# Performance work log

Measured on AMD Instinct MI355X. Metric: run time of the kernel, lower is better.

The kernel has to match this reference:

```python
import jax, jax.numpy as jnp
import numpy as np

N_NODES = 131072
N_EDGES = 2097152
B = 256
NODES_PER_GRAPH = 512  # uniform graphs -> to_dense_batch == reshape
F_IN = 74
D = 128
L = 3
EPS = 1e-5


def setup_inputs() -> dict:
    key = jax.random.key(0)
    ks = jax.random.split(key, 12)
    x = jax.random.normal(ks[0], (N_NODES, F_IN), dtype=jnp.float32)
    edge_index = jax.random.randint(ks[1], (2, N_EDGES), 0, N_NODES, dtype=jnp.int32)
    batch = (jnp.arange(N_NODES, dtype=jnp.int32) // NODES_PER_GRAPH)
    s = 1.0 / np.sqrt(D)
    W_init = jax.random.uniform(ks[2], (F_IN, D), jnp.float32, -s, s)
    W_gcn = jax.random.uniform(ks[3], (L, D, D), jnp.float32, -s, s)
    b_gcn = jnp.zeros((L, D), jnp.float32)
    gamma = jnp.ones((L, D), jnp.float32)
    beta = jnp.zeros((L, D), jnp.float32)
    W_res = jax.random.uniform(ks[4], (L, D, D), jnp.float32, -s, s)
    b_res = jax.random.uniform(ks[5], (L, D), jnp.float32, -s, s)
    return {"x": x, "edge_index": edge_index, "batch": batch, "W_init": W_init,
            "W_gcn": W_gcn, "b_gcn": b_gcn, "gamma": gamma, "beta": beta,
            "W_res": W_res, "b_res": b_res}


def _gcn_conv(x, src, tgt, norm, W, b):
    # PyG GCNConv: h = x @ W ; out[tgt] += norm * h[src] ; + bias
    h = x @ W                                    # [N, D]
    msg = h[src] * norm[:, None]                 # [E+N, D] gather (memory-bound)
    out = jax.ops.segment_sum(msg, tgt, num_segments=N_NODES)
    return out + b


def _batchnorm(x, g, bta):
    mean = jnp.mean(x, axis=0)
    var = jnp.var(x, axis=0)  # biased, matches torch BN training forward
    return (x - mean) * jax.lax.rsqrt(var + EPS) * g + bta


def reference(x, edge_index, batch, W_init, W_gcn, b_gcn, gamma, beta, W_res, b_res):
    # add self loops once; symmetric deg^{-1/2} normalization (PyG default)
    loops = jnp.arange(N_NODES, dtype=edge_index.dtype)
    src = jnp.concatenate([edge_index[0], loops])
    tgt = jnp.concatenate([edge_index[1], loops])
    deg = jax.ops.segment_sum(jnp.ones_like(src, dtype=jnp.float32), tgt,
                              num_segments=N_NODES)
    dinv = jnp.where(deg > 0, jax.lax.rsqrt(jnp.maximum(deg, 1.0)), 0.0)
    norm = dinv[src] * dinv[tgt]

    h = x @ W_init                               # init_transform (no bias)
    for i in range(L):
        conv = _gcn_conv(h, src, tgt, norm, W_gcn[i], b_gcn[i])
        h_new = jax.nn.relu(_batchnorm(conv, gamma[i], beta[i]))
        h = h_new + (h @ W_res[i] + b_res[i])
    # to_dense_batch with uniform NODES_PER_GRAPH -> reshape, all mask=True
    return h.reshape(B, NODES_PER_GRAPH, D)
```

## Files before the change

### kernel.cpp

```cpp
#include <hip/hip_runtime.h>

#define NN 131072
#define NE 2097152
#define DD 128
#define LL 3

#define NB 256
#define BSH 9
#define TILE (NE / NB)

typedef __attribute__((ext_vector_type(8))) short short8;
typedef __attribute__((ext_vector_type(4))) float f32x4;

__device__ __forceinline__ ushort f2bf(float f) {
    uint u = __float_as_uint(f);
    return (ushort)((u + 0x7fffu + ((u >> 16) & 1u)) >> 16);
}
__device__ __forceinline__ float bflo(uint u) { return __uint_as_float(u << 16); }
__device__ __forceinline__ float bfhi(uint u) { return __uint_as_float(u & 0xffff0000u); }

__global__ __launch_bounds__(256) void k_zero(float* __restrict__ bns) {
    int i = blockIdx.x * 256 + threadIdx.x;
    if (i < 768) bns[i] = 0.0f;
}

__global__ __launch_bounds__(256) void kA_count(const int* __restrict__ tgt,
                                                int* __restrict__ blockHist) {
    __shared__ int hist[NB];
    const int t = threadIdx.x, blk = blockIdx.x;
    hist[t] = 0;
    __syncthreads();
    const int base = blk * TILE;
#pragma unroll 8
    for (int j = 0; j < TILE / 256; ++j)
        atomicAdd(&hist[tgt[base + j * 256 + t] >> BSH], 1);
    __syncthreads();
    blockHist[t * NB + blk] = hist[t];
}

__global__ __launch_bounds__(256) void kA_scan(int* __restrict__ blockHist,
                                               int* __restrict__ bstart) {
    __shared__ int part[NB];
    const int t = threadIdx.x;
    int4* bh = (int4*)(blockHist + t * NB);
    int run = 0;
    int4 tmp[NB / 4];
#pragma unroll 8
    for (int j = 0; j < NB / 4; ++j) tmp[j] = bh[j];
#pragma unroll 8
    for (int j = 0; j < NB / 4; ++j) {
        int4 v = tmp[j];
        int a = run; run += v.x;
        int b = run; run += v.y;
        int c = run; run += v.z;
        int d = run; run += v.w;
        tmp[j] = make_int4(a, b, c, d);
    }
    part[t] = run;
    __syncthreads();
    for (int off = 1; off < NB; off <<= 1) {
        int v = part[t];
        int u = (t >= off) ? part[t - off] : 0;
        __syncthreads();
        part[t] = v + u;
        __syncthreads();
    }
    const int excl = part[t] - run;
    bstart[t] = excl;
    if (t == NB - 1) bstart[NB] = part[t];
#pragma unroll 8
    for (int j = 0; j < NB / 4; ++j) {
        int4 v = tmp[j];
        bh[j] = make_int4(v.x + excl, v.y + excl, v.z + excl, v.w + excl);
    }
}

__global__ __launch_bounds__(256) void kA_scatter(const int* __restrict__ src,
                                                  const int* __restrict__ tgt,
                                                  const int* __restrict__ chunkBase,
                                                  uint* __restrict__ packed) {
    __shared__ int cur[NB];
    const int t = threadIdx.x, blk = blockIdx.x;
    cur[t] = chunkBase[t * NB + blk];
    __syncthreads();
    const int base = blk * TILE;
#pragma unroll 4
    for (int j = 0; j < TILE / 256; ++j) {
        const int e = base + j * 256 + t;
        const int tg = tgt[e], s = src[e];
        const int b = tg >> BSH;
        const int pos = atomicAdd(&cur[b], 1);
        packed[pos] = (uint)s | ((uint)(tg & ((1 << BSH) - 1)) << 17);
    }
}

__global__ __launch_bounds__(256) void kB_sort(const uint* __restrict__ packed,
                                               const int* __restrict__ bstart,
                                               int* __restrict__ rowp,
                                               float* __restrict__ dinv,
                                               int* __restrict__ ssrc) {
    __shared__ int cnt[1 << BSH];
    __shared__ int pscan[256];
    const int t = threadIdx.x, b = blockIdx.x;
    const int e0 = bstart[b], e1 = bstart[b + 1];
    cnt[t] = 0; cnt[t + 256] = 0;
    __syncthreads();
    for (int e = e0 + t; e < e1; e += 256)
        atomicAdd(&cnt[packed[e] >> 17], 1);
    __syncthreads();
    const int c0 = cnt[2 * t], c1 = cnt[2 * t + 1];
    pscan[t] = c0 + c1;
    __syncthreads();
    for (int off = 1; off < 256; off <<= 1) {
        int v = pscan[t];
        int u = (t >= off) ? pscan[t - off] : 0;
        __syncthreads();
        pscan[t] = v + u;
        __syncthreads();
    }
    const int ex0 = pscan[t] - c0 - c1;
    const int ex1 = ex0 + c0;
    const int n0 = (b << BSH) + 2 * t;
    rowp[n0] = e0 + ex0;
    rowp[n0 + 1] = e0 + ex1;
    dinv[n0] = rsqrtf((float)(c0 + 1));
    dinv[n0 + 1] = rsqrtf((float)(c1 + 1));
    if (b == NB - 1 && t == 255) rowp[NN] = e1;
    __syncthreads();
    cnt[2 * t] = ex0;
    cnt[2 * t + 1] = ex1;
    __syncthreads();
    for (int e = e0 + t; e < e1; e += 256) {
        const uint p = packed[e];
        const int pos = atomicAdd(&cnt[p >> 17], 1);
        ssrc[e0 + pos] = (int)(p & 0x1FFFFu);
    }
}

__global__ __launch_bounds__(256) void k_prepw(const float* __restrict__ Wi,
                                               const float* __restrict__ Wg,
                                               const float* __restrict__ Wr,
                                               ushort* __restrict__ wt) {
    const int id = blockIdx.x * 256 + threadIdx.x;
    const int m = id >> 14;
    const int c = (id >> 7) & 127;
    const int k = id & 127;
    float v;
    if (m == 0)      v = (k < 74) ? Wi[k * DD + c] : 0.0f;
    else if (m <= 3) v = Wg[(size_t)(m - 1) * DD * DD + k * DD + c];
    else             v = Wr[(size_t)(m - 4) * DD * DD + k * DD + c];
    wt[id] = f2bf(v);
}

__global__ __launch_bounds__(256) void k_convx(const float* __restrict__ x,
                                               uint* __restrict__ xb) {
    const size_t id = (size_t)blockIdx.x * 256 + threadIdx.x;
    const int n = (int)(id >> 6);
    const int k0 = (int)(id & 63) * 2;
    float v0 = (k0 < 74) ? x[(size_t)n * 74 + k0] : 0.0f;
    float v1 = (k0 + 1 < 74) ? x[(size_t)n * 74 + k0 + 1] : 0.0f;
    xb[id] = (uint)f2bf(v0) | ((uint)f2bf(v1) << 16);
}

template <int MODE>
__global__ __launch_bounds__(256) void k_mgemm(const ushort* A,
                                               const ushort* __restrict__ Bt,
                                               ushort* outb,
                                               float* __restrict__ outf,
                                               const float* __restrict__ conv,
                                               const float* __restrict__ ss,
                                               const float* __restrict__ bres,
                                               float* __restrict__ bnsums) {
    __shared__ ushort As[16384];
    __shared__ ushort Bs[16384];
    __shared__ float sred[256];
    const int t = threadIdx.x;
    const int w = t >> 6, l = t & 63;
    const int lc = l & 15, lr = l >> 4;
    const size_t row0 = (size_t)blockIdx.x * 128;

    for (int ch = w * 8; ch < w * 8 + 8; ++ch) {
        const int row = ch * 4 + lr;
        const int kb = (lc * 16) ^ ((row & 7) << 4);
        const ushort* srcA = A + (row0 + row) * DD + (kb >> 1);
        const ushort* srcB = Bt + (size_t)row * DD + (kb >> 1);
        __builtin_amdgcn_global_load_lds(
            (const __attribute__((address_space(1))) void*)srcA,
            (__attribute__((address_space(3))) void*)(As + ch * 512), 16, 0, 0);
        __builtin_amdgcn_global_load_lds(
            (const __attribute__((address_space(1))) void*)srcB,
            (__attribute__((address_space(3))) void*)(Bs + ch * 512), 16, 0, 0);
    }
    if (MODE == 1) sred[t] = 0.0f;
    __syncthreads();

    f32x4 acc[2][8] = {};
    const char* Ab = (const char*)As;
    const char* Bb = (const char*)Bs;
#pragma unroll
    for (int kk = 0; kk < 4; ++kk) {
        const int kb = kk * 64 + lr * 16;
        short8 a[2];
#pragma unroll
        for (int m = 0; m < 2; ++m) {
            const int r = w * 32 + m * 16 + lc;
            a[m] = *(const short8*)(Ab + r * 256 + (kb ^ ((r & 7) << 4)));
        }
#pragma unroll
        for (int n = 0; n < 8; ++n) {
            const int c = n * 16 + lc;
            short8 b = *(const short8*)(Bb + c * 256 + (kb ^ ((c & 7) << 4)));
            acc[0][n] = __builtin_amdgcn_mfma_f32_16x16x32_bf16(a[0], b, acc[0][n], 0, 0, 0);
            acc[1][n] = __builtin_amdgcn_mfma_f32_16x16x32_bf16(a[1], b, acc[1][n], 0, 0, 0);
        }
    }

    if (MODE == 0) {
#pragma unroll
        for (int m = 0; m < 2; ++m)
#pragma unroll
            for (int n = 0; n < 8; ++n) {
                const int c = n * 16 + lc;
#pragma unroll
                for (int j = 0; j < 4; ++j) {
                    const size_t r = row0 + w * 32 + m * 16 + lr * 4 + j;
                    outb[r * DD + c] = f2bf(acc[m][n][j]);
                }
            }
    } else if (MODE == 1) {
#pragma unroll
        for (int n = 0; n < 8; ++n) {
            const int c = n * 16 + lc;
            float ps = 0.0f, ps2 = 0.0f;
#pragma unroll
            for (int m = 0; m < 2; ++m)
#pragma unroll
                for (int j = 0; j < 4; ++j) {
                    const size_t r = row0 + w * 32 + m * 16 + lr * 4 + j;
                    const float v = acc[m][n][j];
                    outf[r * DD + c] = v;
                    ps += v; ps2 += v * v;
                }
            atomicAdd(&sred[c], ps);
            atomicAdd(&sred[DD + c], ps2);
        }
        __syncthreads();
        atomicAdd(&bnsums[t], sred[t]);
    } else {
        float scv[8], shv[8], bbv[8];
#pragma unroll
        for (int n = 0; n < 8; ++n) {
            const int c = n * 16 + lc;
            scv[n] = ss[c]; shv[n] = ss[DD + c]; bbv[n] = bres[c];
        }
#pragma unroll
        for (int m = 0; m < 2; ++m)
#pragma unroll
            for (int n = 0; n < 8; ++n) {
                const int c = n * 16 + lc;
#pragma unroll
                for (int j = 0; j < 4; ++j) {
                    const size_t r = row0 + w * 32 + m * 16 + lr * 4 + j;
                    const float cv = conv[r * DD + c];
                    const float v = fmaxf(cv * scv[n] + shv[n], 0.0f) + acc[m][n][j] + bbv[n];
                    outb[r * DD + c] = f2bf(v);
                    if (MODE == 3) outf[r * DD + c] = v;
                }
            }
    }
}

__global__ __launch_bounds__(256) void k_aggregate(const int* __restrict__ row,
                                                   const int* __restrict__ ssrc,
                                                   const float* __restrict__ dinv,
                                                   const uint* __restrict__ hb,
                                                   uint* __restrict__ aggb) {
    const int n = blockIdx.x * 4 + (threadIdx.x >> 6);
    const int l = threadIdx.x & 63;
    const float dn = dinv[n];
    const uint u = hb[((uint)n << 6) + l];
    const float dn2 = dn * dn;
    float2 acc = make_float2(bflo(u) * dn2, bfhi(u) * dn2);
    const int e0 = row[n], e1 = row[n + 1];
    for (int base = e0; base < e1; base += 64) {
        const int cnt = min(64, e1 - base);
        int sv = 0; float dv = 0.0f;
        if (l < cnt) { sv = ssrc[base + l]; dv = dinv[sv] * dn; }
        for (int i = 0; i < cnt; i += 8) {
            uint vv[8]; float nm[8];
#pragma unroll
            for (int j = 0; j < 8; ++j) {
                const int s = __shfl(sv, i + j);
                nm[j] = __shfl(dv, i + j);
                vv[j] = hb[((uint)s << 6) + l];
            }
#pragma unroll
            for (int j = 0; j < 8; ++j) {
                acc.x += nm[j] * bflo(vv[j]);
                acc.y += nm[j] * bfhi(vv[j]);
            }
        }
    }
    aggb[((uint)n << 6) + l] = (uint)f2bf(acc.x) | ((uint)f2bf(acc.y) << 16);
}

__global__ void k_bnfin(const float* __restrict__ sums,
                        const float* __restrict__ gamma,
                        const float* __restrict__ beta,
                        float* __restrict__ ss) {
    int c = threadIdx.x;
    const float invN = 1.0f / (float)NN;
    float mean = sums[c] * invN;
    float var = sums[DD + c] * invN - mean * mean;
    float sc = gamma[c] * rsqrtf(var + 1e-5f);
    ss[c] = sc;
    ss[DD + c] = beta[c] - mean * sc;
}

extern "C" void kernel_launch(void* const* d_in, const int* in_sizes, int n_in,
                              void* d_out, int out_size, void* d_ws, size_t ws_size,
                              hipStream_t stream) {
    const float* x      = (const float*)d_in[0];
    const int*   ei     = (const int*)d_in[1];
    const float* W_init = (const float*)d_in[3];
    const float* W_gcn  = (const float*)d_in[4];
    const float* gamma  = (const float*)d_in[6];
    const float* beta   = (const float*)d_in[7];
    const float* W_res  = (const float*)d_in[8];
    const float* b_res  = (const float*)d_in[9];

    float* h = (float*)d_out;
    char* p = (char*)d_ws;
    ushort* aggb = (ushort*)p;           p += (size_t)NN * DD * 2;
    ushort* hb  = (ushort*)p;            p += (size_t)NN * DD * 2;
    float*  conv = (float*)p;            p += (size_t)NN * DD * 4;
    uint*   xb   = (uint*)conv;
    float*  dinv = (float*)p;            p += (size_t)NN * 4;
    float*  bns  = (float*)p;            p += 768 * 4;
    float*  ss   = (float*)p;            p += 256 * 4;
    ushort* wt   = (ushort*)p;           p += 7 * 16384 * 2;
    int* blockHist = (int*)p;            p += (size_t)NB * NB * 4;
    int* bstart  = (int*)p;              p += (NB + 1) * 4 + 4;
    uint* packed = (uint*)p;             p += (size_t)NE * 4;
    int* rowp    = (int*)p;              p += ((size_t)NN + 1) * 4 + 4;
    int* ssrc    = (int*)p;

    const int* srcp = ei;
    const int* tgtp = ei + NE;

    k_zero<<<3, 256, 0, stream>>>(bns);
    kA_count<<<NB, 256, 0, stream>>>(tgtp, blockHist);
    kA_scan<<<1, 256, 0, stream>>>(blockHist, bstart);
    kA_scatter<<<NB, 256, 0, stream>>>(srcp, tgtp, blockHist, packed);
    kB_sort<<<NB, 256, 0, stream>>>(packed, bstart, rowp, dinv, ssrc);

    k_prepw<<<7 * 16384 / 256, 256, 0, stream>>>(W_init, W_gcn, W_res, wt);
    k_convx<<<NN * 64 / 256, 256, 0, stream>>>(x, xb);

    k_mgemm<0><<<NN / 128, 256, 0, stream>>>((const ushort*)xb, wt, hb,
                                             nullptr, nullptr, nullptr, nullptr, nullptr);

    for (int i = 0; i < LL; ++i) {
        k_aggregate<<<NN / 4, 256, 0, stream>>>(rowp, ssrc, dinv,
                                                (const uint*)hb, (uint*)aggb);
        k_mgemm<1><<<NN / 128, 256, 0, stream>>>(aggb, wt + (size_t)(1 + i) * 16384,
                                                 nullptr, conv, nullptr, nullptr,
                                                 nullptr, bns + i * 256);
        k_bnfin<<<1, 128, 0, stream>>>(bns + i * 256, gamma + i * DD,
                                       beta + i * DD, ss);
        if (i < LL - 1)
            k_mgemm<2><<<NN / 128, 256, 0, stream>>>(hb, wt + (size_t)(4 + i) * 16384,
                                                     hb, nullptr, conv, ss,
                                                     b_res + i * DD, nullptr);
        else
            k_mgemm<3><<<NN / 128, 256, 0, stream>>>(hb, wt + (size_t)(4 + i) * 16384,
                                                     hb, h, conv, ss,
                                                     b_res + i * DD, nullptr);
    }
}
```

Before: 579.4 us.

## Precompute edge norms, store conv in bf16, fold BN finalize into GEMM

Several changes at once. The three setup kernels are merged into one prep kernel, and the BN finalize kernel is dropped: each residual GEMM block now recomputes scale and shift from the BN sums. The conv output is stored in bf16 instead of fp32, which halves that write and read traffic at some cost in precision. Per-edge normalization is precomputed once into an array, so the aggregation loop no longer gathers dinv[src] or uses shuffles, but it must now stream an extra float per edge each layer.

```diff
diff --git a/kernel.cpp b/kernel.cpp
--- a/kernel.cpp
+++ b/kernel.cpp
@@ -19,9 +19,34 @@
 __device__ __forceinline__ float bflo(uint u) { return __uint_as_float(u << 16); }
 __device__ __forceinline__ float bfhi(uint u) { return __uint_as_float(u & 0xffff0000u); }
 
-__global__ __launch_bounds__(256) void k_zero(float* __restrict__ bns) {
-    int i = blockIdx.x * 256 + threadIdx.x;
-    if (i < 768) bns[i] = 0.0f;
+__global__ __launch_bounds__(256) void k_prep(const float* __restrict__ x,
+                                              const float* __restrict__ Wi,
+                                              const float* __restrict__ Wg,
+                                              const float* __restrict__ Wr,
+                                              uint* __restrict__ xb,
+                                              ushort* __restrict__ wt,
+                                              float* __restrict__ bns) {
+    const int t = threadIdx.x, blk = blockIdx.x;
+    const size_t id = (size_t)blk * 256 + t;
+    const int n = (int)(id >> 6);
+    const int k0 = (int)(id & 63) * 2;
+    float v0 = (k0 < 74) ? x[(size_t)n * 74 + k0] : 0.0f;
+    float v1 = (k0 + 1 < 74) ? x[(size_t)n * 74 + k0 + 1] : 0.0f;
+    xb[id] = (uint)f2bf(v0) | ((uint)f2bf(v1) << 16);
+    if (blk < 448) {
+        const int id2 = blk * 256 + t;
+        const int m = id2 >> 14;
+        const int c = (id2 >> 7) & 127;
+        const int k = id2 & 127;
+        float v;
+        if (m == 0)      v = (k < 74) ? Wi[k * DD + c] : 0.0f;
+        else if (m <= 3) v = Wg[(size_t)(m - 1) * DD * DD + k * DD + c];
+        else             v = Wr[(size_t)(m - 4) * DD * DD + k * DD + c];
+        wt[id2] = f2bf(v);
+    }
+    if (blk == 448) {
+        bns[t] = 0.0f; bns[t + 256] = 0.0f; bns[t + 512] = 0.0f;
+    }
 }
 
 __global__ __launch_bounds__(256) void kA_count(const int* __restrict__ tgt,
@@ -98,9 +123,11 @@
                                                const int* __restrict__ bstart,
                                                int* __restrict__ rowp,
                                                float* __restrict__ dinv,
-                                               int* __restrict__ ssrc) {
+                                               int* __restrict__ ssrc,
+                                               float* __restrict__ nrmf) {
     __shared__ int cnt[1 << BSH];
     __shared__ int pscan[256];
+    __shared__ float dloc[1 << BSH];
     const int t = threadIdx.x, b = blockIdx.x;
     const int e0 = bstart[b], e1 = bstart[b + 1];
     cnt[t] = 0; cnt[t + 256] = 0;
@@ -110,6 +137,8 @@
     __syncthreads();
     const int c0 = cnt[2 * t], c1 = cnt[2 * t + 1];
     pscan[t] = c0 + c1;
+    const float d0 = rsqrtf((float)(c0 + 1)), d1 = rsqrtf((float)(c1 + 1));
+    dloc[2 * t] = d0; dloc[2 * t + 1] = d1;
     __syncthreads();
     for (int off = 1; off < 256; off <<= 1) {
         int v = pscan[t];
@@ -123,8 +152,8 @@
     const int n0 = (b << BSH) + 2 * t;
     rowp[n0] = e0 + ex0;
     rowp[n0 + 1] = e0 + ex1;
-    dinv[n0] = rsqrtf((float)(c0 + 1));
-    dinv[n0 + 1] = rsqrtf((float)(c1 + 1));
+    dinv[n0] = d0;
+    dinv[n0 + 1] = d1;
     if (b == NB - 1 && t == 255) rowp[NN] = e1;
     __syncthreads();
     cnt[2 * t] = ex0;
@@ -132,34 +161,18 @@
     __syncthreads();
     for (int e = e0 + t; e < e1; e += 256) {
         const uint p = packed[e];
-        const int pos = atomicAdd(&cnt[p >> 17], 1);
+        const int tl = p >> 17;
+        const int pos = atomicAdd(&cnt[tl], 1);
         ssrc[e0 + pos] = (int)(p & 0x1FFFFu);
-    }
-}
-
-__global__ __launch_bounds__(256) void k_prepw(const float* __restrict__ Wi,
-                                               const float* __restrict__ Wg,
-                                               const float* __restrict__ Wr,
-                                               ushort* __restrict__ wt) {
-    const int id = blockIdx.x * 256 + threadIdx.x;
-    const int m = id >> 14;
-    const int c = (id >> 7) & 127;
-    const int k = id & 127;
-    float v;
-    if (m == 0)      v = (k < 74) ? Wi[k * DD + c] : 0.0f;
-    else if (m <= 3) v = Wg[(size_t)(m - 1) * DD * DD + k * DD + c];
-    else             v = Wr[(size_t)(m - 4) * DD * DD + k * DD + c];
-    wt[id] = f2bf(v);
-}
-
-__global__ __launch_bounds__(256) void k_convx(const float* __restrict__ x,
-                                               uint* __restrict__ xb) {
-    const size_t id = (size_t)blockIdx.x * 256 + threadIdx.x;
-    const int n = (int)(id >> 6);
-    const int k0 = (int)(id & 63) * 2;
-    float v0 = (k0 < 74) ? x[(size_t)n * 74 + k0] : 0.0f;
-    float v1 = (k0 + 1 < 74) ? x[(size_t)n * 74 + k0 + 1] : 0.0f;
-    xb[id] = (uint)f2bf(v0) | ((uint)f2bf(v1) << 16);
+        nrmf[e0 + pos] = dloc[tl];
+    }
+}
+
+__global__ __launch_bounds__(256) void k_norm(const int* __restrict__ ssrc,
+                                              const float* __restrict__ dinv,
+                                              float* __restrict__ nrmf) {
+    const int e = blockIdx.x * 256 + threadIdx.x;
+    nrmf[e] *= dinv[ssrc[e]];
 }
 
 template <int MODE>
@@ -167,8 +180,9 @@
                                                const ushort* __restrict__ Bt,
                                                ushort* outb,
                                                float* __restrict__ outf,
-                                               const float* __restrict__ conv,
-                                               const float* __restrict__ ss,
+                                               const ushort* __restrict__ convb,
+                                               const float* __restrict__ gamma,
+                                               const float* __restrict__ beta,
                                                const float* __restrict__ bres,
                                                float* __restrict__ bnsums) {
     __shared__ ushort As[16384];
@@ -192,6 +206,14 @@
             (__attribute__((address_space(3))) void*)(Bs + ch * 512), 16, 0, 0);
     }
     if (MODE == 1) sred[t] = 0.0f;
+    if (MODE >= 2 && t < DD) {
+        const float invN = 1.0f / (float)NN;
+        const float mean = bnsums[t] * invN;
+        const float var = bnsums[DD + t] * invN - mean * mean;
+        const float sc = gamma[t] * rsqrtf(var + 1e-5f);
+        sred[t] = sc;
+        sred[DD + t] = beta[t] - mean * sc;
+    }
     __syncthreads();
 
     f32x4 acc[2][8] = {};
@@ -238,7 +260,7 @@
                 for (int j = 0; j < 4; ++j) {
                     const size_t r = row0 + w * 32 + m * 16 + lr * 4 + j;
                     const float v = acc[m][n][j];
-                    outf[r * DD + c] = v;
+                    outb[r * DD + c] = f2bf(v);
                     ps += v; ps2 += v * v;
                 }
             atomicAdd(&sred[c], ps);
@@ -251,7 +273,7 @@
 #pragma unroll
         for (int n = 0; n < 8; ++n) {
             const int c = n * 16 + lc;
-            scv[n] = ss[c]; shv[n] = ss[DD + c]; bbv[n] = bres[c];
+            scv[n] = sred[c]; shv[n] = sred[DD + c]; bbv[n] = bres[c];
         }
 #pragma unroll
         for (int m = 0; m < 2; ++m)
@@ -261,7 +283,7 @@
 #pragma unroll
                 for (int j = 0; j < 4; ++j) {
                     const size_t r = row0 + w * 32 + m * 16 + lr * 4 + j;
-                    const float cv = conv[r * DD + c];
+                    const float cv = __uint_as_float((uint)convb[r * DD + c] << 16);
                     const float v = fmaxf(cv * scv[n] + shv[n], 0.0f) + acc[m][n][j] + bbv[n];
                     outb[r * DD + c] = f2bf(v);
                     if (MODE == 3) outf[r * DD + c] = v;
@@ -270,51 +292,32 @@
     }
 }
 
-__global__ __launch_bounds__(256) void k_aggregate(const int* __restrict__ row,
+__global__ __launch_bounds__(256) void k_aggregate(const int* __restrict__ rowp,
+                                                   const float* __restrict__ dinv,
                                                    const int* __restrict__ ssrc,
-                                                   const float* __restrict__ dinv,
+                                                   const float* __restrict__ nrmf,
                                                    const uint* __restrict__ hb,
                                                    uint* __restrict__ aggb) {
-    const int n = blockIdx.x * 4 + (threadIdx.x >> 6);
+    const int n = __builtin_amdgcn_readfirstlane(blockIdx.x * 4 + (threadIdx.x >> 6));
     const int l = threadIdx.x & 63;
+    const int e0 = rowp[n], e1 = rowp[n + 1];
     const float dn = dinv[n];
-    const uint u = hb[((uint)n << 6) + l];
+    const uint u0 = hb[((uint)n << 6) + l];
     const float dn2 = dn * dn;
-    float2 acc = make_float2(bflo(u) * dn2, bfhi(u) * dn2);
-    const int e0 = row[n], e1 = row[n + 1];
-    for (int base = e0; base < e1; base += 64) {
-        const int cnt = min(64, e1 - base);
-        int sv = 0; float dv = 0.0f;
-        if (l < cnt) { sv = ssrc[base + l]; dv = dinv[sv] * dn; }
-        for (int i = 0; i < cnt; i += 8) {
-            uint vv[8]; float nm[8];
-#pragma unroll
-            for (int j = 0; j < 8; ++j) {
-                const int s = __shfl(sv, i + j);
-                nm[j] = __shfl(dv, i + j);
-                vv[j] = hb[((uint)s << 6) + l];
-            }
-#pragma unroll
-            for (int j = 0; j < 8; ++j) {
-                acc.x += nm[j] * bflo(vv[j]);
-                acc.y += nm[j] * bfhi(vv[j]);
-            }
-        }
-    }
-    aggb[((uint)n << 6) + l] = (uint)f2bf(acc.x) | ((uint)f2bf(acc.y) << 16);
-}
-
-__global__ void k_bnfin(const float* __restrict__ sums,
-                        const float* __restrict__ gamma,
-                        const float* __restrict__ beta,
-                        float* __restrict__ ss) {
-    int c = threadIdx.x;
-    const float invN = 1.0f / (float)NN;
-    float mean = sums[c] * invN;
-    float var = sums[DD + c] * invN - mean * mean;
-    float sc = gamma[c] * rsqrtf(var + 1e-5f);
-    ss[c] = sc;
-    ss[DD + c] = beta[c] - mean * sc;
+    float ax = dn2 * bflo(u0), ay = dn2 * bfhi(u0);
+    for (int e = e0; e < e1; e += 8) {
+#pragma unroll
+        for (int j = 0; j < 8; ++j) {
+            const int idx = min(e + j, e1 - 1);
+            const int s = ssrc[idx];
+            float nm = nrmf[idx];
+            nm = (e + j < e1) ? nm : 0.0f;
+            const uint v = hb[((uint)s << 6) + l];
+            ax += nm * bflo(v);
+            ay += nm * bfhi(v);
+        }
+    }
+    aggb[((uint)n << 6) + l] = (uint)f2bf(ax) | ((uint)f2bf(ay) << 16);
 }
 
 extern "C" void kernel_launch(void* const* d_in, const int* in_sizes, int n_in,
@@ -332,49 +335,48 @@
     float* h = (float*)d_out;
     char* p = (char*)d_ws;
     ushort* aggb = (ushort*)p;           p += (size_t)NN * DD * 2;
-    ushort* hb  = (ushort*)p;            p += (size_t)NN * DD * 2;
-    float*  conv = (float*)p;            p += (size_t)NN * DD * 4;
-    uint*   xb   = (uint*)conv;
+    ushort* hb   = (ushort*)p;           p += (size_t)NN * DD * 2;
+    ushort* convb = (ushort*)p;          p += (size_t)NN * DD * 2;
+    uint*   xb   = (uint*)convb;
     float*  dinv = (float*)p;            p += (size_t)NN * 4;
     float*  bns  = (float*)p;            p += 768 * 4;
-    float*  ss   = (float*)p;            p += 256 * 4;
     ushort* wt   = (ushort*)p;           p += 7 * 16384 * 2;
     int* blockHist = (int*)p;            p += (size_t)NB * NB * 4;
     int* bstart  = (int*)p;              p += (NB + 1) * 4 + 4;
     uint* packed = (uint*)p;             p += (size_t)NE * 4;
     int* rowp    = (int*)p;              p += ((size_t)NN + 1) * 4 + 4;
-    int* ssrc    = (int*)p;
+    int* ssrc    = (int*)p;              p += (size_t)NE * 4;
+    float* nrmf  = (float*)p;            p += (size_t)NE * 4;
 
     const int* srcp = ei;
     const int* tgtp = ei + NE;
 
-    k_zero<<<3, 256, 0, stream>>>(bns);
+    k_prep<<<NN * 64 / 256, 256, 0, stream>>>(x, W_init, W_gcn, W_res, xb, wt, bns);
     kA_count<<<NB, 256, 0, stream>>>(tgtp, blockHist);
     kA_scan<<<1, 256, 0, stream>>>(blockHist, bstart);
     kA_scatter<<<NB, 256, 0, stream>>>(srcp, tgtp, blockHist, packed);
-    kB_sort<<<NB, 256, 0, stream>>>(packed, bstart, rowp, dinv, ssrc);
-
-    k_prepw<<<7 * 16384 / 256, 256, 0, stream>>>(W_init, W_gcn, W_res, wt);
-    k_convx<<<NN * 64 / 256, 256, 0, stream>>>(x, xb);
+    kB_sort<<<NB, 256, 0, stream>>>(packed, bstart, rowp, dinv, ssrc, nrmf);
+    k_norm<<<NE / 256, 256, 0, stream>>>(ssrc, dinv, nrmf);
 
     k_mgemm<0><<<NN / 128, 256, 0, stream>>>((const ushort*)xb, wt, hb,
-                                             nullptr, nullptr, nullptr, nullptr, nullptr);
+                                             nullptr, nullptr, nullptr, nullptr,
+                                             nullptr, nullptr);
 
     for (int i = 0; i < LL; ++i) {
-        k_aggregate<<<NN / 4, 256, 0, stream>>>(rowp, ssrc, dinv,
+        k_aggregate<<<NN / 4, 256, 0, stream>>>(rowp, dinv, ssrc, nrmf,
                                                 (const uint*)hb, (uint*)aggb);
         k_mgemm<1><<<NN / 128, 256, 0, stream>>>(aggb, wt + (size_t)(1 + i) * 16384,
-                                                 nullptr, conv, nullptr, nullptr,
-                                                 nullptr, bns + i * 256);
-        k_bnfin<<<1, 128, 0, stream>>>(bns + i * 256, gamma + i * DD,
-                                       beta + i * DD, ss);
+                                                 convb, nullptr, nullptr, nullptr,
+                                                 nullptr, nullptr, bns + i * 256);
         if (i < LL - 1)
             k_mgemm<2><<<NN / 128, 256, 0, stream>>>(hb, wt + (size_t)(4 + i) * 16384,
-                                                     hb, nullptr, conv, ss,
-                                                     b_res + i * DD, nullptr);
+                                                     hb, nullptr, convb,
+                                                     gamma + i * DD, beta + i * DD,
+                                                     b_res + i * DD, bns + i * 256);
         else
             k_mgemm<3><<<NN / 128, 256, 0, stream>>>(hb, wt + (size_t)(4 + i) * 16384,
-                                                     hb, h, conv, ss,
-                                                     b_res + i * DD, nullptr);
-    }
-}
+                                                     hb, h, convb,
+                                                     gamma + i * DD, beta + i * DD,
+                                                     b_res + i * DD, bns + i * 256);
+    }
+}
```

After: 753.6 us. +30.1%, slower.
